# Performance work log

Measured on AMD Instinct MI355X. Metric: run time of the kernel, lower is better.

Reference implementation:

```python
import jax, jax.numpy as jnp
import numpy as np

B, L, H, NUM_VOCABS = 512, 64, 256, 2046
OUT = NUM_VOCABS + 2


def setup_inputs() -> dict:
    key = jax.random.key(0)
    k1, k2, k3 = jax.random.split(key, 3)
    mol_vec = jax.random.normal(k1, (B, L, H), jnp.float32)
    # parent of node t is a strictly earlier node in the same tree; root (t=0) has none
    rng = np.random.default_rng(0)
    pid = np.zeros((B, L), np.int32)
    for t in range(1, L):
        pid[:, t] = rng.integers(0, t, size=B)
    parent_idx = jnp.asarray(pid)
    Wp = jax.random.normal(k2, (H, H), jnp.float32) * (1.0 / np.sqrt(H))
    bp = jnp.zeros((H,), jnp.float32)
    Wc = jax.random.normal(k3, (H, OUT), jnp.float32) * (1.0 / np.sqrt(H))
    bc = jnp.zeros((OUT,), jnp.float32)
    return dict(mol_vec=mol_vec, parent_idx=parent_idx, Wp=Wp, bp=bp, Wc=Wc, bc=bc)


def _sibling_mean(mol_vec, parent_idx):
    # sibling edges connect nodes sharing a parent; message = mean of siblings' mol_vec
    b, l, h = mol_vec.shape
    seg = parent_idx + jnp.arange(b, dtype=parent_idx.dtype)[:, None] * l  # per-tree parent segment
    seg = jnp.where(jnp.arange(l)[None, :] == 0, b * l, seg)  # roots -> dummy segment
    seg_flat = seg.reshape(-1)
    mv_flat = mol_vec.reshape(-1, h)
    child_sum = jax.ops.segment_sum(mv_flat, seg_flat, num_segments=b * l + 1)
    child_cnt = jax.ops.segment_sum(jnp.ones((b * l,), mol_vec.dtype), seg_flat, num_segments=b * l + 1)
    sib_sum = child_sum[seg_flat] - mv_flat           # exclude self
    sib_cnt = child_cnt[seg_flat] - 1.0
    sib_mean = jnp.where(sib_cnt[:, None] > 0, sib_sum / jnp.maximum(sib_cnt, 1.0)[:, None], 0.0)
    sib_mean = sib_mean.reshape(b, l, h)
    # roots receive no sibling update (their dummy segment is meaningless)
    return jnp.where(jnp.arange(l)[None, :, None] == 0, 0.0, sib_mean)


def _forward(mol_vec, parent_idx, Wp, bp, Wc, bc):
    b, l, h = mol_vec.shape
    sib_mean = _sibling_mean(mol_vec, parent_idx)  # static: mol_vec does not depend on z
    batch_ar = jnp.arange(b)

    def body(z, t):
        # gather parent z (each node has exactly one parent edge; sum == gather)
        pz = z[batch_ar, parent_idx[:, t]]                     # [B, H]
        new = jax.nn.relu(pz @ Wp + bp) + sib_mean[:, t]       # parent_layer + sibling mean
        return z.at[:, t].set(new), None

    z0 = jnp.zeros((b, l, h), mol_vec.dtype)
    z, _ = jax.lax.scan(body, z0, jnp.arange(1, l))
    logits = z.reshape(-1, h) @ Wc + bc                         # classify_layer -> [N, V+2]
    return logits


def reference(mol_vec, parent_idx, Wp, bp, Wc, bc):
    return _forward(mol_vec, parent_idx, Wp, bp, Wc, bc)
```

## Files before the change

### kernel.cpp

```cpp
#include <hip/hip_runtime.h>

#define B_ 512
#define L_ 64
#define H_ 256
#define OUT_ 2048

typedef short bf16x8 __attribute__((ext_vector_type(8)));
typedef float f32x4 __attribute__((ext_vector_type(4)));

static __device__ __forceinline__ unsigned short f2bf(float f) {
  union { float f; unsigned int u; } v; v.f = f;
  unsigned int r = (v.u + 0x7FFFu + ((v.u >> 16) & 1u)) >> 16;
  return (unsigned short)r;
}
static __device__ __forceinline__ float bf2f(unsigned short s) {
  union { unsigned int u; float f; } v; v.u = ((unsigned int)s) << 16;
  return v.f;
}

__global__ __launch_bounds__(256) void pack_kernel(
    const float* __restrict__ Wc, const float* __restrict__ Wp,
    unsigned short* __restrict__ WcB, unsigned short* __restrict__ WpB) {
  int bid = blockIdx.x;
  const float* W;
  unsigned short* dst;
  int ncols, col16;
  if (bid < 128) { W = Wc; dst = WcB; ncols = OUT_; col16 = bid; }
  else           { W = Wp; dst = WpB; ncols = H_;   col16 = bid - 128; }
  int tid = threadIdx.x, l = tid & 63, q = tid >> 6;
  int n = col16 * 16 + (l & 15), g = l >> 4;
#pragma unroll
  for (int kk = 0; kk < 2; ++kk) {
    int kt = q + kk * 4;
    bf16x8 v;
#pragma unroll
    for (int i = 0; i < 8; ++i)
      v[i] = (short)f2bf(W[(size_t)(kt * 32 + g * 8 + i) * ncols + n]);
    *(bf16x8*)&dst[(size_t)(col16 * 8 + kt) * 512 + l * 8] = v;
  }
}

__global__ __launch_bounds__(256, 2) void fused_kernel(
    const float* __restrict__ mol, const int* __restrict__ pidx_g,
    const float* __restrict__ bp, const unsigned short* __restrict__ WpB,
    const unsigned short* __restrict__ WcB, const float* __restrict__ bc,
    float* __restrict__ out) {
  __shared__ unsigned short zbuf[65 * H_];
  __shared__ int pidx[L_];
  __shared__ int cnt_i[64];
  __shared__ unsigned short scale_s[64];
  __shared__ int lvlcnt[64];
  __shared__ int lvlbase[64];
  __shared__ int chkbase[64];
  __shared__ int order_s[64];
  __shared__ int cstart_s[64];
  __shared__ int ccnt_s[64];
  __shared__ int nchunks_s;

  int bid = blockIdx.x;
  int b = bid >> 1, half = bid & 1;
  int tid = threadIdx.x;
  int wv = tid >> 6, l = tid & 63, g = l >> 4, c = l & 15;

  if (tid < 64) pidx[tid] = pidx_g[b * L_ + tid];

  const float* molb = mol + (size_t)b * L_ * H_;
#pragma unroll
  for (int i = 0; i < 8; ++i) {
    int idx = tid + i * 256;
    int t = idx >> 5, h0 = (idx & 31) * 8;
    f32x4 lo = *(const f32x4*)&molb[t * H_ + h0];
    f32x4 hi = *(const f32x4*)&molb[t * H_ + h0 + 4];
    bf16x8 v;
#pragma unroll
    for (int q = 0; q < 4; ++q) { v[q] = (short)f2bf(lo[q]); v[q + 4] = (short)f2bf(hi[q]); }
    *(bf16x8*)&zbuf[(t * H_ + h0) ^ ((t & 7) << 3)] = v;
  }

  if (tid < 64) {
    int t = tid;
    cnt_i[t] = 0;
    lvlcnt[t] = 0;
    int pp = pidx[t];
    if (t >= 1) atomicAdd(&cnt_i[pp], 1);
    int lev = (t == 0) ? 0 : 1;
#pragma unroll
    for (int it = 0; it < 6; ++it) {
      int dp = __shfl(lev, pp);
      int pp2 = __shfl(pp, pp);
      lev += dp;
      pp = pp2;
    }
    int cc = (t >= 1) ? (cnt_i[pidx[t]] - 1) : 0;
    scale_s[t] = (t >= 1 && cc > 0) ? f2bf(1.f / (float)cc) : 0;
    int rank = 0;
    if (t >= 1) rank = atomicAdd(&lvlcnt[lev], 1);
    int lc = lvlcnt[t];
    int nchk = (lc + 15) >> 4;
    int offx = lc, chkx = nchk;
#pragma unroll
    for (int d = 1; d < 64; d <<= 1) {
      int u = __shfl_up(offx, d);
      int v2 = __shfl_up(chkx, d);
      if (t >= d) { offx += u; chkx += v2; }
    }
    lvlbase[t] = offx - lc;
    chkbase[t] = chkx - nchk;
    if (t == 63) nchunks_s = chkx;
    if (t >= 1) {
      int pos = lvlbase[lev] + rank;
      order_s[pos] = t;
      if ((rank & 15) == 0) {
        int cid = chkbase[lev] + (rank >> 4);
        cstart_s[cid] = pos;
        ccnt_s[cid] = min(16, lvlcnt[lev] - rank);
      }
    }
  }
  __syncthreads();

  {
    int pv[2][8];
#pragma unroll
    for (int kt = 0; kt < 2; ++kt)
#pragma unroll
      for (int i = 0; i < 8; ++i) pv[kt][i] = pidx[kt * 32 + g * 8 + i];
    bf16x8 bfr[4][2];
#pragma unroll
    for (int nt = 0; nt < 4; ++nt) {
      int tn = nt * 16 + c;
      int pt = pidx[tn];
      unsigned short scl = scale_s[tn];
#pragma unroll
      for (int kt = 0; kt < 2; ++kt) {
        bf16x8 bv;
#pragma unroll
        for (int i = 0; i < 8; ++i) {
          int tp = kt * 32 + g * 8 + i;
          bv[i] = (tp >= 1 && tp != tn && pv[kt][i] == pt) ? (short)scl : (short)0;
        }
        bfr[nt][kt] = bv;
      }
    }
#pragma unroll
    for (int mtl = 0; mtl < 4; ++mtl) {
      int mtg = wv * 4 + mtl;
      int colh = mtg * 16 + c;
      bf16x8 afr[2];
#pragma unroll
      for (int kt = 0; kt < 2; ++kt) {
        bf16x8 av;
#pragma unroll
        for (int i = 0; i < 8; ++i) {
          int tp = kt * 32 + g * 8 + i;
          av[i] = (short)zbuf[(tp * H_ + colh) ^ ((tp & 7) << 3)];
        }
        afr[kt] = av;
      }
      f32x4 acc4[4] = {};
#pragma unroll
      for (int nt = 0; nt < 4; ++nt)
#pragma unroll
        for (int kt = 0; kt < 2; ++kt)
          acc4[nt] = __builtin_amdgcn_mfma_f32_16x16x32_bf16(afr[kt], bfr[nt][kt], acc4[nt], 0, 0, 0);
#pragma unroll
      for (int nt = 0; nt < 4; ++nt) {
        int ts = nt * 16 + c;
        int swn = (ts & 7) << 3;
#pragma unroll
        for (int j = 0; j < 4; ++j) {
          int h = mtg * 16 + g * 4 + j;
          zbuf[(ts * H_ + h) ^ swn] = f2bf(acc4[nt][j]);
        }
      }
    }
  }

  bf16x8 wfr[4][8];
#pragma unroll
  for (int nt = 0; nt < 4; ++nt)
#pragma unroll
    for (int kt = 0; kt < 8; ++kt)
      wfr[nt][kt] = *(const bf16x8*)&WpB[(size_t)((wv * 4 + nt) * 8 + kt) * 512 + l * 8];
  float bpv[4];
#pragma unroll
  for (int nt = 0; nt < 4; ++nt) bpv[nt] = bp[wv * 64 + nt * 16 + c];
  __syncthreads();

  int nch = nchunks_s;
  for (int ch = 0; ch < nch; ++ch) {
    int cs = cstart_s[ch], cc = ccnt_s[ch];
    int node = (c < cc) ? order_s[cs + c] : 64;
    int par = (node < 64) ? pidx[node] : 0;
    int sp = (par & 7) << 3;
    f32x4 a0 = {0.f, 0.f, 0.f, 0.f};
    f32x4 a1 = {0.f, 0.f, 0.f, 0.f};
    f32x4 a2 = {0.f, 0.f, 0.f, 0.f};
    f32x4 a3 = {0.f, 0.f, 0.f, 0.f};
#pragma unroll
    for (int kt = 0; kt < 8; ++kt) {
      bf16x8 av = *(const bf16x8*)&zbuf[par * H_ + ((kt * 32 + g * 8) ^ sp)];
      a0 = __builtin_amdgcn_mfma_f32_16x16x32_bf16(av, wfr[0][kt], a0, 0, 0, 0);
      a1 = __builtin_amdgcn_mfma_f32_16x16x32_bf16(av, wfr[1][kt], a1, 0, 0, 0);
      a2 = __builtin_amdgcn_mfma_f32_16x16x32_bf16(av, wfr[2][kt], a2, 0, 0, 0);
      a3 = __builtin_amdgcn_mfma_f32_16x16x32_bf16(av, wfr[3][kt], a3, 0, 0, 0);
    }
#pragma unroll
    for (int j = 0; j < 4; ++j) {
      int m = g * 4 + j;
      int nd = (m < cc) ? order_s[cs + m] : 64;
      int swn = (nd & 7) << 3;
      int base = nd * H_ + wv * 64 + c;
      int i0 = (base + 0) ^ swn, i1 = (base + 16) ^ swn;
      int i2 = (base + 32) ^ swn, i3 = (base + 48) ^ swn;
      float v0 = fmaxf(a0[j] + bpv[0], 0.f) + bf2f(zbuf[i0]);
      float v1 = fmaxf(a1[j] + bpv[1], 0.f) + bf2f(zbuf[i1]);
      float v2 = fmaxf(a2[j] + bpv[2], 0.f) + bf2f(zbuf[i2]);
      float v3 = fmaxf(a3[j] + bpv[3], 0.f) + bf2f(zbuf[i3]);
      zbuf[i0] = f2bf(v0);
      zbuf[i1] = f2bf(v1);
      zbuf[i2] = f2bf(v2);
      zbuf[i3] = f2bf(v3);
    }
    __syncthreads();
  }

  bf16x8 areg[4][8];
#pragma unroll
  for (int mt = 0; mt < 4; ++mt) {
    int r = mt * 16 + c;
#pragma unroll
    for (int kt = 0; kt < 8; ++kt)
      areg[mt][kt] = *(const bf16x8*)&zbuf[r * H_ + ((kt * 32 + g * 8) ^ ((r & 7) << 3))];
  }
#pragma unroll 1
  for (int nc = 0; nc < 8; ++nc) {
    int colbase = half * 1024 + nc * 128 + wv * 32;
    float bcv[2];
#pragma unroll
    for (int nt = 0; nt < 2; ++nt) bcv[nt] = bc[colbase + nt * 16 + c];
    f32x4 acc[4][2] = {};
#pragma unroll
    for (int kt = 0; kt < 8; ++kt) {
      bf16x8 bfr[2];
#pragma unroll
      for (int nt = 0; nt < 2; ++nt) {
        int col16 = ((colbase + nt * 16) >> 4);
        bfr[nt] = *(const bf16x8*)&WcB[(size_t)(col16 * 8 + kt) * 512 + l * 8];
      }
#pragma unroll
      for (int nt = 0; nt < 2; ++nt)
#pragma unroll
        for (int mt = 0; mt < 4; ++mt)
          acc[mt][nt] = __builtin_amdgcn_mfma_f32_16x16x32_bf16(
              areg[mt][kt], bfr[nt], acc[mt][nt], 0, 0, 0);
    }
#pragma unroll
    for (int mt = 0; mt < 4; ++mt)
#pragma unroll
      for (int nt = 0; nt < 2; ++nt) {
        int col = colbase + nt * 16 + c;
#pragma unroll
        for (int j = 0; j < 4; ++j) {
          int rt = mt * 16 + g * 4 + j;
          out[(size_t)(b * 64 + rt) * OUT_ + col] = acc[mt][nt][j] + bcv[nt];
        }
      }
  }
}

extern "C" void kernel_launch(void* const* d_in, const int* in_sizes, int n_in,
                              void* d_out, int out_size, void* d_ws, size_t ws_size,
                              hipStream_t stream) {
  const float* mol = (const float*)d_in[0];
  const int* pidx = (const int*)d_in[1];
  const float* Wp = (const float*)d_in[2];
  const float* bp = (const float*)d_in[3];
  const float* Wc = (const float*)d_in[4];
  const float* bc = (const float*)d_in[5];
  float* out = (float*)d_out;

  unsigned short* WcB = (unsigned short*)d_ws;
  unsigned short* WpB = WcB + (size_t)128 * 8 * 512;

  pack_kernel<<<144, 256, 0, stream>>>(Wc, Wp, WcB, WpB);
  fused_kernel<<<2 * B_, 256, 0, stream>>>(mol, pidx, bp, WpB, WcB, bc, out);
}
```

Measured before the change: 99.07 us.

## Merge level-ordered nodes into dependency-respecting chunks across level boundaries

Replaces per-level chunking of the topologically ordered nodes with a greedy serial scan that packs consecutive nodes into chunks of up to 16. A chunk is split only when a node's parent is already inside the current chunk. This cuts the number of sequential chunk steps in the recurrence, since small levels no longer each take a full chunk. In exchange it adds a 63-iteration shuffle loop in setup, run redundantly by one wavefront.

```diff
diff --git a/kernel.cpp b/kernel.cpp
--- a/kernel.cpp
+++ b/kernel.cpp
@@ -51,7 +51,6 @@
   __shared__ unsigned short scale_s[64];
   __shared__ int lvlcnt[64];
   __shared__ int lvlbase[64];
-  __shared__ int chkbase[64];
   __shared__ int order_s[64];
   __shared__ int cstart_s[64];
   __shared__ int ccnt_s[64];
@@ -96,25 +95,37 @@
     int rank = 0;
     if (t >= 1) rank = atomicAdd(&lvlcnt[lev], 1);
     int lc = lvlcnt[t];
-    int nchk = (lc + 15) >> 4;
-    int offx = lc, chkx = nchk;
+    int offx = lc;
 #pragma unroll
     for (int d = 1; d < 64; d <<= 1) {
       int u = __shfl_up(offx, d);
-      int v2 = __shfl_up(chkx, d);
-      if (t >= d) { offx += u; chkx += v2; }
+      if (t >= d) offx += u;
     }
     lvlbase[t] = offx - lc;
-    chkbase[t] = chkx - nchk;
-    if (t == 63) nchunks_s = chkx;
-    if (t >= 1) {
-      int pos = lvlbase[lev] + rank;
-      order_s[pos] = t;
-      if ((rank & 15) == 0) {
-        int cid = chkbase[lev] + (rank >> 4);
-        cstart_s[cid] = pos;
-        ccnt_s[cid] = min(16, lvlcnt[lev] - rank);
-      }
+    if (t >= 1) order_s[lvlbase[lev] + rank] = t;
+
+    int pidv = pidx[t];
+    int ordv = (t < 63) ? order_s[t] : 0;
+    unsigned long long cur = 0;
+    int ck = 0, cstart = 0, cnum = 0;
+    for (int i = 0; i < 63; ++i) {
+      int node = __shfl(ordv, i);
+      int par = __shfl(pidv, node);
+      bool split = (cnum == 16) || ((cur >> par) & 1ull);
+      if (split) {
+        if (t == 0) { cstart_s[ck] = cstart; ccnt_s[ck] = cnum; }
+        ck++;
+        cstart = i;
+        cnum = 0;
+        cur = 0;
+      }
+      cur |= 1ull << node;
+      cnum++;
+    }
+    if (t == 0) {
+      cstart_s[ck] = cstart;
+      ccnt_s[ck] = cnum;
+      nchunks_s = ck + 1;
     }
   }
   __syncthreads();
```

Result: slower. 110.6 us (+11.7%).
